# Kernel optimization log

Measured on AMD Instinct MI355X. Metric: run time of the kernel, lower is better.

Reference implementation:

```python
import jax, jax.numpy as jnp
import numpy as np

N = 16384
D_IN = 64
D_OUT = 64


def setup_inputs() -> dict:
    key = jax.random.key(0)
    k_a, k_x, k_w = jax.random.split(key, 3)
    A = jax.random.uniform(k_a, (N, N), dtype=jnp.float32)  # dense weighted adjacency
    features = jax.random.normal(k_x, (N, D_IN), dtype=jnp.float32)
    weight = jax.random.normal(k_w, (D_IN, D_OUT), dtype=jnp.float32)
    bias = jnp.zeros((D_OUT,), dtype=jnp.float32)
    return {"A": A, "features": features, "weight": weight, "bias": bias}


def reference(A, features, weight, bias):
    # A_hat = A + I ; D = diag(colsum(A_hat)) ; A_norm = D^{-1} A_hat D^{-1}
    # Exploit diagonal D: two-sided scaling instead of inverse + dense matmuls.
    d_inv = 1.0 / (jnp.sum(A, axis=0) + 1.0)          # [N]
    xs = features * d_inv[:, None]                     # right-scale: D^{-1} x
    agg = (A @ xs + xs) * d_inv[:, None]               # (A + I) xs, then left-scale
    # dropout keep-prob = 1 - (1 - self.dropout) = 1.0 -> identity (dropout=1.0)
    return jax.nn.relu(agg @ weight + bias)
```

## Files before the change

### kernel.cpp

```cpp
#include <hip/hip_runtime.h>
#include <hip/hip_bf16.h>
#include <cstdint>
#include <cstddef>

#define N 16384
#define DF 64

typedef __attribute__((ext_vector_type(8))) short short8;
typedef __attribute__((ext_vector_type(4))) float f32x4;

__device__ __forceinline__ unsigned short f2bf(float f) {
    union { float f; uint32_t u; } v; v.f = f;
    uint32_t u = v.u;
    uint32_t r = u + 0x7fffu + ((u >> 16) & 1u);
    return (unsigned short)(r >> 16);
}

#define PROWS 64
__global__ __launch_bounds__(256) void colsum_kernel(const float* __restrict__ A,
                                                     float* __restrict__ partial) {
    int t = threadIdx.x;
    int c0 = blockIdx.x * 1024 + t * 4;
    int r0 = blockIdx.y * 256;
    const float* p = A + (size_t)r0 * N + c0;
    float ax = 0.f, ay = 0.f, az = 0.f, aw = 0.f;
    #pragma unroll 8
    for (int r = 0; r < 256; ++r) {
        float4 v = *(const float4*)(p + (size_t)r * N);
        ax += v.x; ay += v.y; az += v.z; aw += v.w;
    }
    float4 o; o.x = ax; o.y = ay; o.z = az; o.w = aw;
    *(float4*)&partial[(size_t)blockIdx.y * N + c0] = o;
}

__global__ __launch_bounds__(256) void prep_kernel(const float* __restrict__ feat,
                                                   const float* __restrict__ partial,
                                                   float* __restrict__ d_inv,
                                                   unsigned short* __restrict__ xsT) {
    __shared__ float tile[64][68];
    int t = threadIdx.x;
    int i0 = blockIdx.x * 64;
    int r = t >> 2;
    int q = t & 3;
    float s = 0.f;
    #pragma unroll
    for (int p = 0; p < 16; ++p)
        s += partial[(size_t)(q * 16 + p) * N + i0 + r];
    s += __shfl_xor(s, 1);
    s += __shfl_xor(s, 2);
    float dinv = 1.0f / (s + 1.0f);
    if (q == 0) d_inv[i0 + r] = dinv;

    int cq = q * 16;
    const float* fp = feat + (size_t)(i0 + r) * DF + cq;
    #pragma unroll
    for (int j = 0; j < 16; j += 4) {
        float4 v = *(const float4*)(fp + j);
        tile[r][cq + j + 0] = v.x * dinv;
        tile[r][cq + j + 1] = v.y * dinv;
        tile[r][cq + j + 2] = v.z * dinv;
        tile[r][cq + j + 3] = v.w * dinv;
    }
    __syncthreads();
    int c = t >> 2;
    int iq = (t & 3) * 16;
    short8 b0, b1;
    #pragma unroll
    for (int j = 0; j < 8; ++j) b0[j] = (short)f2bf(tile[iq + j][c]);
    #pragma unroll
    for (int j = 0; j < 8; ++j) b1[j] = (short)f2bf(tile[iq + 8 + j][c]);
    unsigned short* dst = xsT + (size_t)c * N + i0 + iq;
    *(short8*)(dst) = b0;
    *(short8*)(dst + 8) = b1;
}

#define KSPLIT 8
#define KCHUNK (N / KSPLIT)
#define BK 128
#define LDK 136

__global__ __launch_bounds__(256, 8) void gemm_kernel(const float* __restrict__ A,
                                                      const unsigned short* __restrict__ xsT,
                                                      float* __restrict__ agg) {
    __shared__ __align__(16) unsigned short xtile[64 * LDK];
    int t = threadIdx.x;
    int bid = blockIdx.x;
    int mb = bid >> 3;
    int ks = bid & 7;
    int m0 = mb * 64;
    int k0 = ks * KCHUNK;
    int w = t >> 6;
    int l = t & 63;
    int row = m0 + w * 16 + (l & 15);
    int kofs = (l >> 4) * 8;

    const float* arow = A + (size_t)row * N + k0 + kofs;

    f32x4 acc[4] = {};

    for (int kt = 0; kt < KCHUNK; kt += BK) {
        __syncthreads();
        #pragma unroll
        for (int i = 0; i < 4; ++i) {
            int ch = t + i * 256;
            int c = ch >> 4;
            int ko = (ch & 15) * 8;
            *(short8*)&xtile[c * LDK + ko] =
                *(const short8*)&xsT[(size_t)c * N + k0 + kt + ko];
        }
        __syncthreads();
        #pragma unroll
        for (int kk = 0; kk < BK; kk += 32) {
            float4 a0 = *(const float4*)(arow + kt + kk);
            float4 a1 = *(const float4*)(arow + kt + kk + 4);
            short8 af;
            af[0] = (short)f2bf(a0.x); af[1] = (short)f2bf(a0.y);
            af[2] = (short)f2bf(a0.z); af[3] = (short)f2bf(a0.w);
            af[4] = (short)f2bf(a1.x); af[5] = (short)f2bf(a1.y);
            af[6] = (short)f2bf(a1.z); af[7] = (short)f2bf(a1.w);
            #pragma unroll
            for (int ct = 0; ct < 4; ++ct) {
                short8 bf = *(const short8*)&xtile[(ct * 16 + (l & 15)) * LDK + kk + kofs];
                acc[ct] = __builtin_amdgcn_mfma_f32_16x16x32_bf16(af, bf, acc[ct], 0, 0, 0);
            }
        }
    }
    float* slab = agg + (size_t)ks * N * DF;
    int crow = m0 + w * 16 + (l >> 4) * 4;
    int ccol = l & 15;
    #pragma unroll
    for (int ct = 0; ct < 4; ++ct) {
        #pragma unroll
        for (int q = 0; q < 4; ++q)
            slab[(size_t)(crow + q) * DF + ct * 16 + ccol] = acc[ct][q];
    }
}

__global__ __launch_bounds__(256) void epilogue_kernel(const float* __restrict__ agg,
                                                       const float* __restrict__ feat,
                                                       const float* __restrict__ d_inv,
                                                       const float* __restrict__ W,
                                                       const float* __restrict__ bias,
                                                       float* __restrict__ out) {
    __shared__ float aggL[64][65];
    __shared__ float wL[64][64];
    int t = threadIdx.x;
    int i0 = blockIdx.x * 64;
    int r = t >> 2;
    int cq = (t & 3) * 16;
    {
        const float* wp = W + r * 64 + cq;
        #pragma unroll
        for (int j = 0; j < 16; j += 4) {
            float4 v = *(const float4*)(wp + j);
            wL[r][cq + j + 0] = v.x; wL[r][cq + j + 1] = v.y;
            wL[r][cq + j + 2] = v.z; wL[r][cq + j + 3] = v.w;
        }
    }
    float dinv = d_inv[i0 + r];
    const float* fp = feat + (size_t)(i0 + r) * DF + cq;
    size_t base = (size_t)(i0 + r) * DF + cq;
    #pragma unroll
    for (int j = 0; j < 16; j += 4) {
        float4 fv = *(const float4*)(fp + j);
        float sx = fv.x * dinv, sy = fv.y * dinv, sz = fv.z * dinv, sw = fv.w * dinv;
        #pragma unroll
        for (int sl = 0; sl < KSPLIT; ++sl) {
            float4 a = *(const float4*)(agg + (size_t)sl * N * DF + base + j);
            sx += a.x; sy += a.y; sz += a.z; sw += a.w;
        }
        aggL[r][cq + j + 0] = sx * dinv;
        aggL[r][cq + j + 1] = sy * dinv;
        aggL[r][cq + j + 2] = sz * dinv;
        aggL[r][cq + j + 3] = sw * dinv;
    }
    __syncthreads();
    int k = t & 63;
    int rg = t >> 6;
    float bk = bias[k];
    for (int it = 0; it < 16; ++it) {
        int rr = rg * 16 + it;
        float acc = bk;
        #pragma unroll
        for (int c = 0; c < 64; ++c) acc += aggL[rr][c] * wL[c][k];
        out[(size_t)(i0 + rr) * DF + k] = fmaxf(acc, 0.0f);
    }
}

extern "C" void kernel_launch(void* const* d_in, const int* in_sizes, int n_in,
                              void* d_out, int out_size, void* d_ws, size_t ws_size,
                              hipStream_t stream) {
    const float* A    = (const float*)d_in[0];
    const float* feat = (const float*)d_in[1];
    const float* W    = (const float*)d_in[2];
    const float* bias = (const float*)d_in[3];
    float* out = (float*)d_out;

    float* ws = (float*)d_ws;
    float* partial = ws;
    float* agg     = ws + (size_t)PROWS * N;
    float* dinv    = agg + (size_t)KSPLIT * N * DF;
    unsigned short* xsT = (unsigned short*)(dinv + N);

    colsum_kernel<<<dim3(16, 64), 256, 0, stream>>>(A, partial);
    prep_kernel<<<N / 64, 256, 0, stream>>>(feat, partial, dinv, xsT);
    gemm_kernel<<<(N / 64) * KSPLIT, 256, 0, stream>>>(A, xsT, agg);
    epilogue_kernel<<<N / 64, 256, 0, stream>>>(agg, feat, dinv, W, bias, out);
}
```

Baseline: 430.9 us.

## Chunk colsum/prep/GEMM by column blocks so GEMM rereads A from cache

```diff
diff --git a/kernel.cpp b/kernel.cpp
--- a/kernel.cpp
+++ b/kernel.cpp
@@ -5,6 +5,10 @@
 
 #define N 16384
 #define DF 64
+#define CHUNK 2048
+#define NCHUNK (N / CHUNK)
+#define KSUB 1024
+#define NSLAB (N / KSUB)
 
 typedef __attribute__((ext_vector_type(8))) short short8;
 typedef __attribute__((ext_vector_type(4))) float f32x4;
@@ -16,43 +20,47 @@
     return (unsigned short)(r >> 16);
 }
 
-#define PROWS 64
-__global__ __launch_bounds__(256) void colsum_kernel(const float* __restrict__ A,
-                                                     float* __restrict__ partial) {
-    int t = threadIdx.x;
-    int c0 = blockIdx.x * 1024 + t * 4;
-    int r0 = blockIdx.y * 256;
+__global__ __launch_bounds__(256) void colsum_chunk_kernel(const float* __restrict__ A,
+                                                           float* __restrict__ partial,
+                                                           int chunk) {
+    int t = threadIdx.x;
+    int cl = blockIdx.x * 1024 + t * 4;
+    int c0 = chunk * CHUNK + cl;
+    int r0 = blockIdx.y * 64;
     const float* p = A + (size_t)r0 * N + c0;
     float ax = 0.f, ay = 0.f, az = 0.f, aw = 0.f;
     #pragma unroll 8
-    for (int r = 0; r < 256; ++r) {
+    for (int r = 0; r < 64; ++r) {
         float4 v = *(const float4*)(p + (size_t)r * N);
         ax += v.x; ay += v.y; az += v.z; aw += v.w;
     }
     float4 o; o.x = ax; o.y = ay; o.z = az; o.w = aw;
-    *(float4*)&partial[(size_t)blockIdx.y * N + c0] = o;
-}
-
-__global__ __launch_bounds__(256) void prep_kernel(const float* __restrict__ feat,
-                                                   const float* __restrict__ partial,
-                                                   float* __restrict__ d_inv,
-                                                   unsigned short* __restrict__ xsT) {
+    *(float4*)&partial[(size_t)blockIdx.y * CHUNK + cl] = o;
+}
+
+__global__ __launch_bounds__(256) void prep_chunk_kernel(const float* __restrict__ feat,
+                                                         const float* __restrict__ partial,
+                                                         float* __restrict__ d_inv,
+                                                         unsigned short* __restrict__ xsT,
+                                                         int chunk) {
+    __shared__ float sums[4][64];
     __shared__ float tile[64][68];
     int t = threadIdx.x;
-    int i0 = blockIdx.x * 64;
-    int r = t >> 2;
-    int q = t & 3;
+    int w = t >> 6, l = t & 63;
+    int kl0 = blockIdx.x * 64;
+    int k0 = chunk * CHUNK + kl0;
     float s = 0.f;
-    #pragma unroll
-    for (int p = 0; p < 16; ++p)
-        s += partial[(size_t)(q * 16 + p) * N + i0 + r];
-    s += __shfl_xor(s, 1);
-    s += __shfl_xor(s, 2);
-    float dinv = 1.0f / (s + 1.0f);
-    if (q == 0) d_inv[i0 + r] = dinv;
+    #pragma unroll 8
+    for (int p = 0; p < 64; ++p)
+        s += partial[(size_t)(w * 64 + p) * CHUNK + kl0 + l];
+    sums[w][l] = s;
+    __syncthreads();
+    int r = t >> 2, q = t & 3;
+    float dinv = 1.0f / (sums[0][r] + sums[1][r] + sums[2][r] + sums[3][r] + 1.0f);
+    if (q == 0) d_inv[k0 + r] = dinv;
 
     int cq = q * 16;
-    const float* fp = feat + (size_t)(i0 + r) * DF + cq;
+    const float* fp = feat + (size_t)(k0 + r) * DF + cq;
     #pragma unroll
     for (int j = 0; j < 16; j += 4) {
         float4 v = *(const float4*)(fp + j);
@@ -62,33 +70,31 @@
         tile[r][cq + j + 3] = v.w * dinv;
     }
     __syncthreads();
-    int c = t >> 2;
+    int f = t >> 2;
     int iq = (t & 3) * 16;
     short8 b0, b1;
     #pragma unroll
-    for (int j = 0; j < 8; ++j) b0[j] = (short)f2bf(tile[iq + j][c]);
-    #pragma unroll
-    for (int j = 0; j < 8; ++j) b1[j] = (short)f2bf(tile[iq + 8 + j][c]);
-    unsigned short* dst = xsT + (size_t)c * N + i0 + iq;
+    for (int j = 0; j < 8; ++j) b0[j] = (short)f2bf(tile[iq + j][f]);
+    #pragma unroll
+    for (int j = 0; j < 8; ++j) b1[j] = (short)f2bf(tile[iq + 8 + j][f]);
+    unsigned short* dst = xsT + (size_t)f * N + k0 + iq;
     *(short8*)(dst) = b0;
     *(short8*)(dst + 8) = b1;
 }
 
-#define KSPLIT 8
-#define KCHUNK (N / KSPLIT)
 #define BK 128
 #define LDK 136
 
-__global__ __launch_bounds__(256, 8) void gemm_kernel(const float* __restrict__ A,
-                                                      const unsigned short* __restrict__ xsT,
-                                                      float* __restrict__ agg) {
+__global__ __launch_bounds__(256, 8) void gemm_chunk_kernel(const float* __restrict__ A,
+                                                            const unsigned short* __restrict__ xsT,
+                                                            float* __restrict__ agg,
+                                                            int chunk) {
     __shared__ __align__(16) unsigned short xtile[64 * LDK];
     int t = threadIdx.x;
-    int bid = blockIdx.x;
-    int mb = bid >> 3;
-    int ks = bid & 7;
+    int mb = blockIdx.x >> 1;
+    int ksub = blockIdx.x & 1;
     int m0 = mb * 64;
-    int k0 = ks * KCHUNK;
+    int k0 = chunk * CHUNK + ksub * KSUB;
     int w = t >> 6;
     int l = t & 63;
     int row = m0 + w * 16 + (l & 15);
@@ -98,15 +104,15 @@
 
     f32x4 acc[4] = {};
 
-    for (int kt = 0; kt < KCHUNK; kt += BK) {
+    for (int kt = 0; kt < KSUB; kt += BK) {
         __syncthreads();
         #pragma unroll
         for (int i = 0; i < 4; ++i) {
             int ch = t + i * 256;
-            int c = ch >> 4;
+            int f = ch >> 4;
             int ko = (ch & 15) * 8;
-            *(short8*)&xtile[c * LDK + ko] =
-                *(const short8*)&xsT[(size_t)c * N + k0 + kt + ko];
+            *(short8*)&xtile[f * LDK + ko] =
+                *(const short8*)&xsT[(size_t)f * N + k0 + kt + ko];
         }
         __syncthreads();
         #pragma unroll
@@ -125,7 +131,7 @@
             }
         }
     }
-    float* slab = agg + (size_t)ks * N * DF;
+    float* slab = agg + (size_t)(chunk * 2 + ksub) * N * DF;
     int crow = m0 + w * 16 + (l >> 4) * 4;
     int ccol = l & 15;
     #pragma unroll
@@ -165,7 +171,7 @@
         float4 fv = *(const float4*)(fp + j);
         float sx = fv.x * dinv, sy = fv.y * dinv, sz = fv.z * dinv, sw = fv.w * dinv;
         #pragma unroll
-        for (int sl = 0; sl < KSPLIT; ++sl) {
+        for (int sl = 0; sl < NSLAB; ++sl) {
             float4 a = *(const float4*)(agg + (size_t)sl * N * DF + base + j);
             sx += a.x; sy += a.y; sz += a.z; sw += a.w;
         }
@@ -198,12 +204,14 @@
 
     float* ws = (float*)d_ws;
     float* partial = ws;
-    float* agg     = ws + (size_t)PROWS * N;
-    float* dinv    = agg + (size_t)KSPLIT * N * DF;
+    float* agg     = ws + (size_t)256 * CHUNK;
+    float* dinv    = agg + (size_t)NSLAB * N * DF;
     unsigned short* xsT = (unsigned short*)(dinv + N);
 
-    colsum_kernel<<<dim3(16, 64), 256, 0, stream>>>(A, partial);
-    prep_kernel<<<N / 64, 256, 0, stream>>>(feat, partial, dinv, xsT);
-    gemm_kernel<<<(N / 64) * KSPLIT, 256, 0, stream>>>(A, xsT, agg);
+    for (int c = 0; c < NCHUNK; ++c) {
+        colsum_chunk_kernel<<<dim3(2, 256), 256, 0, stream>>>(A, partial, c);
+        prep_chunk_kernel<<<CHUNK / 64, 256, 0, stream>>>(feat, partial, dinv, xsT, c);
+        gemm_chunk_kernel<<<512, 256, 0, stream>>>(A, xsT, agg, c);
+    }
     epilogue_kernel<<<N / 64, 256, 0, stream>>>(agg, feat, dinv, W, bias, out);
 }
```

Result: slower. 624.5 us (+45.0%).

## Stage A tile through swizzled LDS with contiguous 128-byte row loads

Applied to the files above, without the earlier changes.

```diff
diff --git a/kernel.cpp b/kernel.cpp
--- a/kernel.cpp
+++ b/kernel.cpp
@@ -79,10 +79,11 @@
 #define BK 128
 #define LDK 136
 
-__global__ __launch_bounds__(256, 8) void gemm_kernel(const float* __restrict__ A,
+__global__ __launch_bounds__(256, 4) void gemm_kernel(const float* __restrict__ A,
                                                       const unsigned short* __restrict__ xsT,
                                                       float* __restrict__ agg) {
     __shared__ __align__(16) unsigned short xtile[64 * LDK];
+    __shared__ __align__(16) unsigned short atile[64 * BK];
     int t = threadIdx.x;
     int bid = blockIdx.x;
     int mb = bid >> 3;
@@ -91,10 +92,18 @@
     int k0 = ks * KCHUNK;
     int w = t >> 6;
     int l = t & 63;
-    int row = m0 + w * 16 + (l & 15);
-    int kofs = (l >> 4) * 8;
-
-    const float* arow = A + (size_t)row * N + k0 + kofs;
+
+    int srow = t >> 2;
+    int sq = t & 3;
+    const float* asrc = A + (size_t)(m0 + srow) * N + k0 + sq * 32;
+    const int abyte_w = srow * (BK * 2) + sq * 64;
+    const int aswz_w = (srow & 7) << 4;
+
+    int fr = l & 15;
+    int fq = l >> 4;
+    int arow_l = w * 16 + fr;
+    const int abyte_r = arow_l * (BK * 2) + fq * 16;
+    const int aswz_r = (arow_l & 7) << 4;
 
     f32x4 acc[4] = {};
 
@@ -103,24 +112,51 @@
         #pragma unroll
         for (int i = 0; i < 4; ++i) {
             int ch = t + i * 256;
-            int c = ch >> 4;
+            int f = ch >> 4;
             int ko = (ch & 15) * 8;
-            *(short8*)&xtile[c * LDK + ko] =
-                *(const short8*)&xsT[(size_t)c * N + k0 + kt + ko];
+            *(short8*)&xtile[f * LDK + ko] =
+                *(const short8*)&xsT[(size_t)f * N + k0 + kt + ko];
+        }
+        {
+            float4 v0 = *(const float4*)(asrc + kt + 0);
+            float4 v1 = *(const float4*)(asrc + kt + 4);
+            float4 v2 = *(const float4*)(asrc + kt + 8);
+            float4 v3 = *(const float4*)(asrc + kt + 12);
+            float4 v4 = *(const float4*)(asrc + kt + 16);
+            float4 v5 = *(const float4*)(asrc + kt + 20);
+            float4 v6 = *(const float4*)(asrc + kt + 24);
+            float4 v7 = *(const float4*)(asrc + kt + 28);
+            short8 o0, o1, o2, o3;
+            o0[0] = (short)f2bf(v0.x); o0[1] = (short)f2bf(v0.y);
+            o0[2] = (short)f2bf(v0.z); o0[3] = (short)f2bf(v0.w);
+            o0[4] = (short)f2bf(v1.x); o0[5] = (short)f2bf(v1.y);
+            o0[6] = (short)f2bf(v1.z); o0[7] = (short)f2bf(v1.w);
+            o1[0] = (short)f2bf(v2.x); o1[1] = (short)f2bf(v2.y);
+            o1[2] = (short)f2bf(v2.z); o1[3] = (short)f2bf(v2.w);
+            o1[4] = (short)f2bf(v3.x); o1[5] = (short)f2bf(v3.y);
+            o1[6] = (short)f2bf(v3.z); o1[7] = (short)f2bf(v3.w);
+            o2[0] = (short)f2bf(v4.x); o2[1] = (short)f2bf(v4.y);
+            o2[2] = (short)f2bf(v4.z); o2[3] = (short)f2bf(v4.w);
+            o2[4] = (short)f2bf(v5.x); o2[5] = (short)f2bf(v5.y);
+            o2[6] = (short)f2bf(v5.z); o2[7] = (short)f2bf(v5.w);
+            o3[0] = (short)f2bf(v6.x); o3[1] = (short)f2bf(v6.y);
+            o3[2] = (short)f2bf(v6.z); o3[3] = (short)f2bf(v6.w);
+            o3[4] = (short)f2bf(v7.x); o3[5] = (short)f2bf(v7.y);
+            o3[6] = (short)f2bf(v7.z); o3[7] = (short)f2bf(v7.w);
+            char* ab = (char*)atile;
+            *(short8*)(ab + (((abyte_w + 0)  ^ aswz_w))) = o0;
+            *(short8*)(ab + (((abyte_w + 16) ^ aswz_w))) = o1;
+            *(short8*)(ab + (((abyte_w + 32) ^ aswz_w))) = o2;
+            *(short8*)(ab + (((abyte_w + 48) ^ aswz_w))) = o3;
         }
         __syncthreads();
+        const char* abr = (const char*)atile;
         #pragma unroll
         for (int kk = 0; kk < BK; kk += 32) {
-            float4 a0 = *(const float4*)(arow + kt + kk);
-            float4 a1 = *(const float4*)(arow + kt + kk + 4);
-            short8 af;
-            af[0] = (short)f2bf(a0.x); af[1] = (short)f2bf(a0.y);
-            af[2] = (short)f2bf(a0.z); af[3] = (short)f2bf(a0.w);
-            af[4] = (short)f2bf(a1.x); af[5] = (short)f2bf(a1.y);
-            af[6] = (short)f2bf(a1.z); af[7] = (short)f2bf(a1.w);
+            short8 af = *(const short8*)(abr + ((abyte_r + kk * 2) ^ aswz_r));
             #pragma unroll
             for (int ct = 0; ct < 4; ++ct) {
-                short8 bf = *(const short8*)&xtile[(ct * 16 + (l & 15)) * LDK + kk + kofs];
+                short8 bf = *(const short8*)&xtile[(ct * 16 + fr) * LDK + kk + fq * 8];
                 acc[ct] = __builtin_amdgcn_mfma_f32_16x16x32_bf16(af, bf, acc[ct], 0, 0, 0);
             }
         }
```

New measurement: 460.3 us. 6.8% more time.

## Double-buffer xs tile and prefetch A into registers in GEMM loop

Applied to the files above, without the earlier changes.

```diff
diff --git a/kernel.cpp b/kernel.cpp
--- a/kernel.cpp
+++ b/kernel.cpp
@@ -77,12 +77,13 @@
 #define KSPLIT 8
 #define KCHUNK (N / KSPLIT)
 #define BK 128
+#define NT (KCHUNK / BK)
 #define LDK 136
 
-__global__ __launch_bounds__(256, 8) void gemm_kernel(const float* __restrict__ A,
+__global__ __launch_bounds__(256, 4) void gemm_kernel(const float* __restrict__ A,
                                                       const unsigned short* __restrict__ xsT,
                                                       float* __restrict__ agg) {
-    __shared__ __align__(16) unsigned short xtile[64 * LDK];
+    __shared__ __align__(16) unsigned short xtile[2][64 * LDK];
     int t = threadIdx.x;
     int bid = blockIdx.x;
     int mb = bid >> 3;
@@ -91,37 +92,92 @@
     int k0 = ks * KCHUNK;
     int w = t >> 6;
     int l = t & 63;
-    int row = m0 + w * 16 + (l & 15);
-    int kofs = (l >> 4) * 8;
-
-    const float* arow = A + (size_t)row * N + k0 + kofs;
+    int fr = l & 15;
+    int fq = l >> 4;
+    int row = m0 + w * 16 + fr;
+    const float* arow = A + (size_t)row * N + k0 + fq * 8;
+
+    int f0 = t >> 4;
+    int ko = (t & 15) * 8;
+    const unsigned short* bsrc = xsT + (size_t)f0 * N + k0 + ko;
 
     f32x4 acc[4] = {};
-
-    for (int kt = 0; kt < KCHUNK; kt += BK) {
-        __syncthreads();
-        #pragma unroll
-        for (int i = 0; i < 4; ++i) {
-            int ch = t + i * 256;
-            int c = ch >> 4;
-            int ko = (ch & 15) * 8;
-            *(short8*)&xtile[c * LDK + ko] =
-                *(const short8*)&xsT[(size_t)c * N + k0 + kt + ko];
-        }
-        __syncthreads();
-        #pragma unroll
-        for (int kk = 0; kk < BK; kk += 32) {
-            float4 a0 = *(const float4*)(arow + kt + kk);
-            float4 a1 = *(const float4*)(arow + kt + kk + 4);
-            short8 af;
-            af[0] = (short)f2bf(a0.x); af[1] = (short)f2bf(a0.y);
-            af[2] = (short)f2bf(a0.z); af[3] = (short)f2bf(a0.w);
-            af[4] = (short)f2bf(a1.x); af[5] = (short)f2bf(a1.y);
-            af[6] = (short)f2bf(a1.z); af[7] = (short)f2bf(a1.w);
+    short8 sreg[4];
+    float4 ar[8];
+    short8 abf[4];
+
+    #pragma unroll
+    for (int i = 0; i < 4; ++i)
+        sreg[i] = *(const short8*)(bsrc + (size_t)i * 16 * N);
+    #pragma unroll
+    for (int s = 0; s < 4; ++s) {
+        ar[2 * s]     = *(const float4*)(arow + s * 32);
+        ar[2 * s + 1] = *(const float4*)(arow + s * 32 + 4);
+    }
+    #pragma unroll
+    for (int i = 0; i < 4; ++i)
+        *(short8*)&xtile[0][(f0 + i * 16) * LDK + ko] = sreg[i];
+    #pragma unroll
+    for (int s = 0; s < 4; ++s) {
+        short8 o;
+        o[0] = (short)f2bf(ar[2*s].x);   o[1] = (short)f2bf(ar[2*s].y);
+        o[2] = (short)f2bf(ar[2*s].z);   o[3] = (short)f2bf(ar[2*s].w);
+        o[4] = (short)f2bf(ar[2*s+1].x); o[5] = (short)f2bf(ar[2*s+1].y);
+        o[6] = (short)f2bf(ar[2*s+1].z); o[7] = (short)f2bf(ar[2*s+1].w);
+        abf[s] = o;
+    }
+    asm volatile("s_waitcnt lgkmcnt(0)" ::: "memory");
+    __builtin_amdgcn_s_barrier();
+
+    int cur = 0;
+    for (int tt = 0; tt < NT - 1; ++tt) {
+        int kt2 = (tt + 1) * BK;
+        #pragma unroll
+        for (int i = 0; i < 4; ++i)
+            sreg[i] = *(const short8*)(bsrc + (size_t)i * 16 * N + kt2);
+        #pragma unroll
+        for (int s = 0; s < 4; ++s) {
+            ar[2 * s]     = *(const float4*)(arow + kt2 + s * 32);
+            ar[2 * s + 1] = *(const float4*)(arow + kt2 + s * 32 + 4);
+        }
+        {
+            const unsigned short* xr = &xtile[cur][0];
+            #pragma unroll
+            for (int s = 0; s < 4; ++s) {
+                #pragma unroll
+                for (int ct = 0; ct < 4; ++ct) {
+                    short8 bf = *(const short8*)&xr[(ct * 16 + fr) * LDK + s * 32 + fq * 8];
+                    acc[ct] = __builtin_amdgcn_mfma_f32_16x16x32_bf16(abf[s], bf, acc[ct], 0, 0, 0);
+                }
+            }
+        }
+        {
+            unsigned short* xwd = &xtile[cur ^ 1][0];
+            #pragma unroll
+            for (int i = 0; i < 4; ++i)
+                *(short8*)&xwd[(f0 + i * 16) * LDK + ko] = sreg[i];
+        }
+        #pragma unroll
+        for (int s = 0; s < 4; ++s) {
+            short8 o;
+            o[0] = (short)f2bf(ar[2*s].x);   o[1] = (short)f2bf(ar[2*s].y);
+            o[2] = (short)f2bf(ar[2*s].z);   o[3] = (short)f2bf(ar[2*s].w);
+            o[4] = (short)f2bf(ar[2*s+1].x); o[5] = (short)f2bf(ar[2*s+1].y);
+            o[6] = (short)f2bf(ar[2*s+1].z); o[7] = (short)f2bf(ar[2*s+1].w);
+            abf[s] = o;
+        }
+        asm volatile("s_waitcnt lgkmcnt(0)" ::: "memory");
+        __builtin_amdgcn_s_barrier();
+        cur ^= 1;
+    }
+    {
+        const unsigned short* xr = &xtile[cur][0];
+        #pragma unroll
+        for (int s = 0; s < 4; ++s) {
             #pragma unroll
             for (int ct = 0; ct < 4; ++ct) {
-                short8 bf = *(const short8*)&xtile[(ct * 16 + (l & 15)) * LDK + kk + kofs];
-                acc[ct] = __builtin_amdgcn_mfma_f32_16x16x32_bf16(af, bf, acc[ct], 0, 0, 0);
+                short8 bf = *(const short8*)&xr[(ct * 16 + fr) * LDK + s * 32 + fq * 8];
+                acc[ct] = __builtin_amdgcn_mfma_f32_16x16x32_bf16(abf[s], bf, acc[ct], 0, 0, 0);
             }
         }
     }
```

Result: slower. 441.4 us (+2.4%).
